# Optimization experiments

Hardware: AMD Instinct MI355X
Metric: run time of the kernel (lower is better)

## Reference

```python
import jax, jax.numpy as jnp
import numpy as np

NUM_EMBED = 1024
HEAD_SIZE = 64
B, T = 4, 4096

def setup_inputs() -> dict:
    key = jax.random.key(0)
    kx, kq, kk, kv = jax.random.split(key, 4)
    scale = NUM_EMBED ** -0.5
    return {
        "x": jax.random.normal(kx, (B, T, NUM_EMBED), dtype=jnp.float32),
        "Wq": jax.random.normal(kq, (NUM_EMBED, HEAD_SIZE), dtype=jnp.float32) * scale,
        "Wk": jax.random.normal(kk, (NUM_EMBED, HEAD_SIZE), dtype=jnp.float32) * scale,
        "Wv": jax.random.normal(kv, (NUM_EMBED, HEAD_SIZE), dtype=jnp.float32) * scale,
    }

def reference(x, Wq, Wk, Wv):
    # x: [B,T,C]; Wq/Wk/Wv: [C,H]
    q = jnp.einsum('btc,ch->bth', x, Wq)
    k = jnp.einsum('btc,ch->bth', x, Wk)
    v = jnp.einsum('btc,ch->bth', x, Wv)
    Tq = x.shape[1]
    att = jnp.einsum('bth,bsh->bts', q, k) * (k.shape[-1] ** -0.5)  # [B,T,T]
    causal = jnp.tril(jnp.ones((Tq, Tq), dtype=bool))
    att = jnp.where(causal, att, -jnp.inf)
    att = jax.nn.softmax(att, axis=-1)
    # dropout p=0 (eval mode): identity
    out = jnp.einsum('bts,bsh->bth', att, v)  # [B,T,H]
    return out
```

## Files before the change

kernel.cpp:

```cpp
#include <hip/hip_runtime.h>

#define B_ 4
#define T_ 4096
#define C_ 1024
#define H_ 64

typedef _Float16 half8  __attribute__((ext_vector_type(8)));
typedef _Float16 half4_ __attribute__((ext_vector_type(4)));
typedef float    floatx4 __attribute__((ext_vector_type(4)));

#define MFMA16(a, b, c) __builtin_amdgcn_mfma_f32_16x16x32_f16(a, b, c, 0, 0, 0)

__global__ __launch_bounds__(256) void pack_w_kn(
    const float* __restrict__ Wq, const float* __restrict__ Wk,
    const float* __restrict__ Wv, _Float16* __restrict__ Wt2)
{
    const int idx  = blockIdx.x * 256 + threadIdx.x;
    const int mt   = idx >> 14;
    const int j    = (idx >> 10) & 15;
    const int f    = (idx >> 9) & 1;
    const int lane = (idx >> 3) & 63;
    const int jj   = idx & 7;
    const int q = lane >> 4, c = lane & 15;
    const int k  = j * 64 + f * 32 + q * 8 + jj;
    const int hp = mt * 16 + c;
    const float* W = (hp < 64) ? Wq : (hp < 128) ? Wk : Wv;
    Wt2[idx] = (_Float16)W[k * H_ + (hp & 63)];
}

__global__ __launch_bounds__(512) void qkv_kn(
    const float* __restrict__ x, const _Float16* __restrict__ Wt2,
    _Float16* __restrict__ Qh, _Float16* __restrict__ Kpk,
    _Float16* __restrict__ Vpk)
{
    __shared__ _Float16 xs[2][32][72];
    const int tid  = threadIdx.x;
    const int lane = tid & 63, w = tid >> 6;
    const int q    = lane >> 4, c = lane & 15;
    const int nt   = w & 1;
    const int mg   = w >> 1;
    const int row0 = blockIdx.x * 32;

    const int srow = tid >> 4, scol = (tid & 15) * 4;
    const float* xg = x + (size_t)(row0 + srow) * C_ + scol;

    floatx4 acc[3];
    #pragma unroll
    for (int i = 0; i < 3; ++i) acc[i] = floatx4{0.f, 0.f, 0.f, 0.f};

    float4 g = *(const float4*)xg;

    for (int j = 0; j < 16; ++j) {
        half4_ hv;
        hv[0] = (_Float16)g.x; hv[1] = (_Float16)g.y;
        hv[2] = (_Float16)g.z; hv[3] = (_Float16)g.w;
        *(half4_*)(&xs[j & 1][srow][scol]) = hv;
        __syncthreads();
        if (j < 15) g = *(const float4*)(xg + (j + 1) * 64);

        const _Float16* xrow = &xs[j & 1][nt * 16 + c][q * 8];
        const half8 b0 = *(const half8*)xrow;
        const half8 b1 = *(const half8*)(xrow + 32);

        half8 a[6];
        #pragma unroll
        for (int i = 0; i < 3; ++i) {
            const size_t fb = ((size_t)((mg * 3 + i) * 16 + j) * 2) * 512 + lane * 8;
            a[i * 2]     = *(const half8*)(Wt2 + fb);
            a[i * 2 + 1] = *(const half8*)(Wt2 + fb + 512);
        }
        #pragma unroll
        for (int i = 0; i < 3; ++i) {
            acc[i] = MFMA16(a[i * 2],     b0, acc[i]);
            acc[i] = MFMA16(a[i * 2 + 1], b1, acc[i]);
        }
    }

    const int row = row0 + nt * 16 + c;
    const int b = row >> 12, t4 = row & (T_ - 1);
    const int kt = t4 >> 6;
    const size_t tbase = ((size_t)b * 64 + kt) * 4096;
    const int mtk = (t4 >> 4) & 3;
    const int kk  = t4 & 63;

    #pragma unroll
    for (int i = 0; i < 3; ++i) {
        const int gi = mg * 3 + i;
        if (gi < 4) {
            half4_ v;
            #pragma unroll
            for (int r = 0; r < 4; ++r) v[r] = (_Float16)acc[i][r];
            *(half4_*)(Qh + (size_t)row * H_ + gi * 16 + q * 4) = v;
        } else if (gi < 8) {
            half4_ v;
            #pragma unroll
            for (int r = 0; r < 4; ++r) v[r] = (_Float16)acc[i][r];
            const int e  = gi - 4;
            const int f  = e >> 1;
            const int qa = (e * 2 + (q >> 1)) & 3;
            *(half4_*)(Kpk + tbase + ((size_t)(mtk * 2 + f) * 64 + qa * 16 + c) * 8
                       + (q & 1) * 4) = v;
        } else {
            const int mtv = gi - 8;
            const int qa = (kk >> 3) & 3, fv = kk >> 5, jv = kk & 7;
            #pragma unroll
            for (int r = 0; r < 4; ++r) {
                const int cv = q * 4 + r;
                Vpk[tbase + ((size_t)(mtv * 2 + fv) * 64 + qa * 16 + cv) * 8 + jv]
                    = (_Float16)acc[i][r];
            }
        }
    }
}

__global__ __launch_bounds__(512, 4) void attn_kn(
    const _Float16* __restrict__ Qh, const _Float16* __restrict__ Kpk,
    const _Float16* __restrict__ Vpk, float* __restrict__ out)
{
    __shared__ __align__(16) char smem[73728];
    const int lane = threadIdx.x & 63;
    const int w    = threadIdx.x >> 6;
    const int q    = lane >> 4, c = lane & 15;

    const int bid  = blockIdx.x;
    const int xcd  = bid & 7;
    const int slot = bid >> 3;
    const int b    = xcd >> 1;
    const int t32  = 127 - ((slot << 1) | (xcd & 1));

    const int row0 = t32 * 32;
    const int grow = b * T_ + row0;
    const int nk   = (t32 >> 1) + 1;

    _Float16* Pw = (_Float16*)smem + w * 4608;

    const _Float16 qs = (_Float16)0.18033688f;
    half8 bq0[2], bq1[2];
    #pragma unroll
    for (int g = 0; g < 2; ++g) {
        const _Float16* qb = Qh + (size_t)(grow + g * 16 + c) * H_;
        bq0[g] = *(const half8*)(qb + q * 8);
        bq1[g] = *(const half8*)(qb + 32 + q * 8);
        bq0[g] *= qs; bq1[g] *= qs;
    }

    floatx4 o[4][2];
    #pragma unroll
    for (int i = 0; i < 4; ++i)
        #pragma unroll
        for (int g = 0; g < 2; ++g) o[i][g] = floatx4{0.f, 0.f, 0.f, 0.f};
    float m[2] = {-3.0e38f, -3.0e38f}, l[2] = {0.f, 0.f};

    for (int kt = w; kt < nk; kt += 8) {
        const int kb = kt * 64;
        const _Float16* Kt = Kpk + ((size_t)b * 64 + kt) * 4096;
        const _Float16* Vt = Vpk + ((size_t)b * 64 + kt) * 4096;
        half8 a0[4], a1[4];

        #pragma unroll
        for (int mt = 0; mt < 4; ++mt) {
            a0[mt] = *(const half8*)(Kt + ((size_t)(mt * 2)     * 64 + lane) * 8);
            a1[mt] = *(const half8*)(Kt + ((size_t)(mt * 2 + 1) * 64 + lane) * 8);
        }
        floatx4 s[4][2];
        #pragma unroll
        for (int mt = 0; mt < 4; ++mt)
            #pragma unroll
            for (int g = 0; g < 2; ++g) {
                floatx4 z = floatx4{0.f, 0.f, 0.f, 0.f};
                z = MFMA16(a0[mt], bq0[g], z);
                s[mt][g] = MFMA16(a1[mt], bq1[g], z);
            }
        #pragma unroll
        for (int mt = 0; mt < 4; ++mt) {
            a0[mt] = *(const half8*)(Vt + ((size_t)(mt * 2)     * 64 + lane) * 8);
            a1[mt] = *(const half8*)(Vt + ((size_t)(mt * 2 + 1) * 64 + lane) * 8);
        }

        if (kt == nk - 1) {
            #pragma unroll
            for (int mt = 0; mt < 4; ++mt)
                #pragma unroll
                for (int g = 0; g < 2; ++g)
                    #pragma unroll
                    for (int r = 0; r < 4; ++r)
                        if (kb + mt * 16 + q * 4 + r > row0 + g * 16 + c)
                            s[mt][g][r] = -3.0e38f;
        }

        _Float16* Pb = Pw + ((kt >> 3) & 1) * 2304;
        #pragma unroll
        for (int g = 0; g < 2; ++g) {
            float mx = s[0][g][0];
            #pragma unroll
            for (int mt = 0; mt < 4; ++mt)
                #pragma unroll
                for (int r = 0; r < 4; ++r) mx = fmaxf(mx, s[mt][g][r]);
            mx = fmaxf(mx, __shfl_xor(mx, 16, 64));
            mx = fmaxf(mx, __shfl_xor(mx, 32, 64));
            const float mn    = fmaxf(m[g], mx);
            const float alpha = exp2f(m[g] - mn);
            _Float16* pl = Pb + g * 1152 + c * 72;
            float sl = 0.f;
            #pragma unroll
            for (int mt = 0; mt < 4; ++mt) {
                half4_ ph;
                #pragma unroll
                for (int r = 0; r < 4; ++r) {
                    const float e = exp2f(s[mt][g][r] - mn);
                    sl += e;
                    ph[r] = (_Float16)e;
                }
                *(half4_*)(pl + mt * 16 + q * 4) = ph;
            }
            sl += __shfl_xor(sl, 16, 64);
            sl += __shfl_xor(sl, 32, 64);
            l[g] = l[g] * alpha + sl;
            m[g] = mn;
            #pragma unroll
            for (int mt = 0; mt < 4; ++mt) o[mt][g] *= alpha;
        }

        half8 bp0[2], bp1[2];
        #pragma unroll
        for (int g = 0; g < 2; ++g) {
            const _Float16* pl = Pb + g * 1152 + c * 72;
            bp0[g] = *(const half8*)(pl + q * 8);
            bp1[g] = *(const half8*)(pl + 32 + q * 8);
        }
        #pragma unroll
        for (int mt = 0; mt < 4; ++mt)
            #pragma unroll
            for (int g = 0; g < 2; ++g) {
                o[mt][g] = MFMA16(a0[mt], bp0[g], o[mt][g]);
                o[mt][g] = MFMA16(a1[mt], bp1[g], o[mt][g]);
            }
    }

    __syncthreads();
    float* Ol = (float*)smem;
    float* Ml = (float*)(smem + 69632);
    float* Ll = (float*)(smem + 70656);
    if (q == 0) { Ml[w * 32 + c] = m[0]; Ml[w * 32 + 16 + c] = m[1]; }
    __syncthreads();
    float M0 = Ml[c], M1 = Ml[16 + c];
    #pragma unroll
    for (int w2 = 1; w2 < 8; ++w2) {
        M0 = fmaxf(M0, Ml[w2 * 32 + c]);
        M1 = fmaxf(M1, Ml[w2 * 32 + 16 + c]);
    }
    const float alpha0 = exp2f(m[0] - M0);
    const float alpha1 = exp2f(m[1] - M1);
    if (q == 0) { Ll[w * 32 + c] = l[0] * alpha0; Ll[w * 32 + 16 + c] = l[1] * alpha1; }
    #pragma unroll
    for (int mt = 0; mt < 4; ++mt)
        #pragma unroll
        for (int r = 0; r < 4; ++r) {
            Ol[w * 2176 + (mt * 16 + q * 4 + r) * 17 + c]        = o[mt][0][r] * alpha0;
            Ol[w * 2176 + (64 + mt * 16 + q * 4 + r) * 17 + c]   = o[mt][1][r] * alpha1;
        }
    __syncthreads();

    const int g  = w & 1;
    const int h0 = (w >> 1) * 16 + q * 4;
    float L = 0.f;
    #pragma unroll
    for (int w2 = 0; w2 < 8; ++w2) L += Ll[w2 * 32 + g * 16 + c];
    const float inv = 1.f / L;
    floatx4 st = floatx4{0.f, 0.f, 0.f, 0.f};
    #pragma unroll
    for (int w2 = 0; w2 < 8; ++w2)
        #pragma unroll
        for (int r = 0; r < 4; ++r)
            st[r] += Ol[w2 * 2176 + (g * 64 + h0 + r) * 17 + c];
    st *= inv;
    *(floatx4*)(out + (size_t)(grow + g * 16 + c) * H_ + h0) = st;
}

extern "C" void kernel_launch(void* const* d_in, const int* in_sizes, int n_in,
                              void* d_out, int out_size, void* d_ws, size_t ws_size,
                              hipStream_t stream) {
    const float* x  = (const float*)d_in[0];
    const float* Wq = (const float*)d_in[1];
    const float* Wk = (const float*)d_in[2];
    const float* Wv = (const float*)d_in[3];
    float* out = (float*)d_out;

    _Float16* ws = (_Float16*)d_ws;
    _Float16* Wt2 = ws;
    _Float16* Qh  = ws + 196608;
    _Float16* Kpk = Qh + 1048576;
    _Float16* Vpk = Kpk + 1048576;

    hipLaunchKernelGGL(pack_w_kn, dim3(768), dim3(256), 0, stream, Wq, Wk, Wv, Wt2);
    hipLaunchKernelGGL(qkv_kn, dim3((B_ * T_) / 32), dim3(512), 0, stream,
                       x, Wt2, Qh, Kpk, Vpk);
    hipLaunchKernelGGL(attn_kn, dim3(512), dim3(512), 0, stream,
                       Qh, Kpk, Vpk, out);
}
```

Measured before the change: 171.1 us.

## Feed softmax probabilities to PV MFMA from registers, halve LDS, rebalance causal blocks

The attention kernel now passes the exp'd probabilities straight from the QK^T accumulator layout into 16x16x16 MFMAs as the B operand, so P is no longer written to and read back from LDS. V is repacked in the projection kernel to match that operand layout. The final cross-wave reduction is split into two passes over half-size buffers, which halves shared memory and may raise occupancy. The block-to-tile mapping also interleaves long and short causal rows differently to balance work. The cost is twice as many smaller MFMA instructions and an extra barrier in the epilogue.

```diff
diff --git a/kernel.cpp b/kernel.cpp
--- a/kernel.cpp
+++ b/kernel.cpp
@@ -9,7 +9,10 @@
 typedef _Float16 half4_ __attribute__((ext_vector_type(4)));
 typedef float    floatx4 __attribute__((ext_vector_type(4)));
 
-#define MFMA16(a, b, c) __builtin_amdgcn_mfma_f32_16x16x32_f16(a, b, c, 0, 0, 0)
+#define MFMA16(a, b, c)  __builtin_amdgcn_mfma_f32_16x16x32_f16(a, b, c, 0, 0, 0)
+#define MFMA16K(a, b, c) __builtin_amdgcn_mfma_f32_16x16x16f16(a, b, c, 0, 0, 0)
+#define LO4(v) __builtin_shufflevector(v, v, 0, 1, 2, 3)
+#define HI4(v) __builtin_shufflevector(v, v, 4, 5, 6, 7)
 
 __global__ __launch_bounds__(256) void pack_w_kn(
     const float* __restrict__ Wq, const float* __restrict__ Wk,
@@ -102,12 +105,15 @@
                        + (q & 1) * 4) = v;
         } else {
             const int mtv = gi - 8;
-            const int qa = (kk >> 3) & 3, fv = kk >> 5, jv = kk & 7;
+            const int qa2 = (kk >> 2) & 3;
+            const int h4  = (kk >> 4) & 1;
+            const int f2  = kk >> 5;
+            const int i2  = kk & 3;
             #pragma unroll
             for (int r = 0; r < 4; ++r) {
                 const int cv = q * 4 + r;
-                Vpk[tbase + ((size_t)(mtv * 2 + fv) * 64 + qa * 16 + cv) * 8 + jv]
-                    = (_Float16)acc[i][r];
+                Vpk[tbase + ((size_t)(mtv * 2 + f2) * 64 + qa2 * 16 + cv) * 8
+                    + h4 * 4 + i2] = (_Float16)acc[i][r];
             }
         }
     }
@@ -117,7 +123,7 @@
     const _Float16* __restrict__ Qh, const _Float16* __restrict__ Kpk,
     const _Float16* __restrict__ Vpk, float* __restrict__ out)
 {
-    __shared__ __align__(16) char smem[73728];
+    __shared__ __align__(16) char smem[36864];
     const int lane = threadIdx.x & 63;
     const int w    = threadIdx.x >> 6;
     const int q    = lane >> 4, c = lane & 15;
@@ -126,13 +132,13 @@
     const int xcd  = bid & 7;
     const int slot = bid >> 3;
     const int b    = xcd >> 1;
-    const int t32  = 127 - ((slot << 1) | (xcd & 1));
+    const int e    = xcd & 1;
+    const int t32  = (slot < 32) ? (127 - (2 * slot + e))
+                                 : (2 * (slot - 32) + e);
 
     const int row0 = t32 * 32;
     const int grow = b * T_ + row0;
     const int nk   = (t32 >> 1) + 1;
-
-    _Float16* Pw = (_Float16*)smem + w * 4608;
 
     const _Float16 qs = (_Float16)0.18033688f;
     half8 bq0[2], bq1[2];
@@ -188,7 +194,7 @@
                             s[mt][g][r] = -3.0e38f;
         }
 
-        _Float16* Pb = Pw + ((kt >> 3) & 1) * 2304;
+        half4_ ph[2][4];
         #pragma unroll
         for (int g = 0; g < 2; ++g) {
             float mx = s[0][g][0];
@@ -200,19 +206,15 @@
             mx = fmaxf(mx, __shfl_xor(mx, 32, 64));
             const float mn    = fmaxf(m[g], mx);
             const float alpha = exp2f(m[g] - mn);
-            _Float16* pl = Pb + g * 1152 + c * 72;
             float sl = 0.f;
             #pragma unroll
-            for (int mt = 0; mt < 4; ++mt) {
-                half4_ ph;
+            for (int mt = 0; mt < 4; ++mt)
                 #pragma unroll
                 for (int r = 0; r < 4; ++r) {
-                    const float e = exp2f(s[mt][g][r] - mn);
-                    sl += e;
-                    ph[r] = (_Float16)e;
+                    const float ev = exp2f(s[mt][g][r] - mn);
+                    sl += ev;
+                    ph[g][mt][r] = (_Float16)ev;
                 }
-                *(half4_*)(pl + mt * 16 + q * 4) = ph;
-            }
             sl += __shfl_xor(sl, 16, 64);
             sl += __shfl_xor(sl, 32, 64);
             l[g] = l[g] * alpha + sl;
@@ -221,26 +223,26 @@
             for (int mt = 0; mt < 4; ++mt) o[mt][g] *= alpha;
         }
 
-        half8 bp0[2], bp1[2];
-        #pragma unroll
-        for (int g = 0; g < 2; ++g) {
-            const _Float16* pl = Pb + g * 1152 + c * 72;
-            bp0[g] = *(const half8*)(pl + q * 8);
-            bp1[g] = *(const half8*)(pl + 32 + q * 8);
-        }
-        #pragma unroll
-        for (int mt = 0; mt < 4; ++mt)
+        #pragma unroll
+        for (int mt = 0; mt < 4; ++mt) {
+            const half4_ v0 = LO4(a0[mt]);
+            const half4_ v1 = HI4(a0[mt]);
+            const half4_ v2 = LO4(a1[mt]);
+            const half4_ v3 = HI4(a1[mt]);
             #pragma unroll
             for (int g = 0; g < 2; ++g) {
-                o[mt][g] = MFMA16(a0[mt], bp0[g], o[mt][g]);
-                o[mt][g] = MFMA16(a1[mt], bp1[g], o[mt][g]);
+                o[mt][g] = MFMA16K(v0, ph[g][0], o[mt][g]);
+                o[mt][g] = MFMA16K(v1, ph[g][1], o[mt][g]);
+                o[mt][g] = MFMA16K(v2, ph[g][2], o[mt][g]);
+                o[mt][g] = MFMA16K(v3, ph[g][3], o[mt][g]);
             }
-    }
-
+        }
+    }
+
+    float* Ol = (float*)smem;
+    float* Ml = (float*)(smem + 34816);
+    float* Ll = (float*)(smem + 35840);
     __syncthreads();
-    float* Ol = (float*)smem;
-    float* Ml = (float*)(smem + 69632);
-    float* Ll = (float*)(smem + 70656);
     if (q == 0) { Ml[w * 32 + c] = m[0]; Ml[w * 32 + 16 + c] = m[1]; }
     __syncthreads();
     float M0 = Ml[c], M1 = Ml[16 + c];
@@ -252,29 +254,31 @@
     const float alpha0 = exp2f(m[0] - M0);
     const float alpha1 = exp2f(m[1] - M1);
     if (q == 0) { Ll[w * 32 + c] = l[0] * alpha0; Ll[w * 32 + 16 + c] = l[1] * alpha1; }
-    #pragma unroll
-    for (int mt = 0; mt < 4; ++mt)
-        #pragma unroll
-        for (int r = 0; r < 4; ++r) {
-            Ol[w * 2176 + (mt * 16 + q * 4 + r) * 17 + c]        = o[mt][0][r] * alpha0;
-            Ol[w * 2176 + (64 + mt * 16 + q * 4 + r) * 17 + c]   = o[mt][1][r] * alpha1;
-        }
-    __syncthreads();
-
-    const int g  = w & 1;
-    const int h0 = (w >> 1) * 16 + q * 4;
-    float L = 0.f;
-    #pragma unroll
-    for (int w2 = 0; w2 < 8; ++w2) L += Ll[w2 * 32 + g * 16 + c];
-    const float inv = 1.f / L;
-    floatx4 st = floatx4{0.f, 0.f, 0.f, 0.f};
-    #pragma unroll
-    for (int w2 = 0; w2 < 8; ++w2)
-        #pragma unroll
-        for (int r = 0; r < 4; ++r)
-            st[r] += Ol[w2 * 2176 + (g * 64 + h0 + r) * 17 + c];
-    st *= inv;
-    *(floatx4*)(out + (size_t)(grow + g * 16 + c) * H_ + h0) = st;
+
+    const int h0 = w * 8 + q * 2;
+    #pragma unroll
+    for (int gp = 0; gp < 2; ++gp) {
+        const float a = gp ? alpha1 : alpha0;
+        #pragma unroll
+        for (int mt = 0; mt < 4; ++mt)
+            #pragma unroll
+            for (int r = 0; r < 4; ++r)
+                Ol[w * 1088 + (mt * 16 + q * 4 + r) * 17 + c] = o[mt][gp][r] * a;
+        __syncthreads();
+        float L = 0.f;
+        #pragma unroll
+        for (int w2 = 0; w2 < 8; ++w2) L += Ll[w2 * 32 + gp * 16 + c];
+        const float inv = 1.f / L;
+        float ox = 0.f, oy = 0.f;
+        #pragma unroll
+        for (int w2 = 0; w2 < 8; ++w2) {
+            ox += Ol[w2 * 1088 + h0 * 17 + c];
+            oy += Ol[w2 * 1088 + (h0 + 1) * 17 + c];
+        }
+        float2 st; st.x = ox * inv; st.y = oy * inv;
+        *(float2*)(out + (size_t)(grow + gp * 16 + c) * H_ + h0) = st;
+        if (gp == 0) __syncthreads();
+    }
 }
 
 extern "C" void kernel_launch(void* const* d_in, const int* in_sizes, int n_in,
```

Result: faster. 165.5 us (-3.2%).
